# Kernel optimization log

Measured on AMD Instinct MI355X. Metric: run time of the kernel, lower is better.

The kernel has to match this reference:

```python
import jax, jax.numpy as jnp
import numpy as np

STATE_DIM = 512
N_AGENTS = 16
N_ACTIONS = 32
EMBED = 512          # mixing_embed_dim
Q_IN = STATE_DIM + N_AGENTS * N_ACTIONS  # 1024 (coma_critic arch)
ROWS = 32768         # bs * ts = 64 * 512


def _linear_params(key, d_in, d_out):
    kw, kb = jax.random.split(key)
    bound = 1.0 / np.sqrt(d_in)
    W = jax.random.uniform(kw, (d_in, d_out), minval=-bound, maxval=bound, dtype=jnp.float32)
    b = jax.random.uniform(kb, (d_out,), minval=-bound, maxval=bound, dtype=jnp.float32)
    return W, b


def setup_inputs() -> dict:
    key = jax.random.key(0)
    ks = jax.random.split(key, 8)
    states = jax.random.normal(ks[0], (ROWS, STATE_DIM), dtype=jnp.float32)
    actions = jax.random.uniform(ks[1], (ROWS, N_AGENTS * N_ACTIONS), dtype=jnp.float32)
    Qw1, Qb1 = _linear_params(ks[2], Q_IN, EMBED)
    Qw2, Qb2 = _linear_params(ks[3], EMBED, EMBED)
    Qw3, Qb3 = _linear_params(ks[4], EMBED, 1)
    Vw1, Vb1 = _linear_params(ks[5], STATE_DIM, EMBED)
    Vw2, Vb2 = _linear_params(ks[6], EMBED, EMBED)
    Vw3, Vb3 = _linear_params(ks[7], EMBED, 1)
    return {
        "states": states, "actions": actions,
        "Qw1": Qw1, "Qb1": Qb1, "Qw2": Qw2, "Qb2": Qb2, "Qw3": Qw3, "Qb3": Qb3,
        "Vw1": Vw1, "Vb1": Vb1, "Vw2": Vw2, "Vb2": Vb2, "Vw3": Vw3, "Vb3": Vb3,
    }


def _mlp3(x, W1, b1, W2, b2, W3, b3):
    h = jax.nn.relu(x @ W1 + b1)
    h = jax.nn.relu(h @ W2 + b2)
    return h @ W3 + b3


def reference(states, actions,
              Qw1, Qb1, Qw2, Qb2, Qw3, Qb3,
              Vw1, Vb1, Vw2, Vb2, Vw3, Vb3):
    # coma_critic arch: inputs = cat([states, joint-action one-hots], dim=1)
    inputs = jnp.concatenate([states, actions], axis=1)  # [bs*ts, Q_IN]
    q_outputs = _mlp3(inputs, Qw1, Qb1, Qw2, Qb2, Qw3, Qb3)  # [bs*ts, 1]
    v_outputs = _mlp3(states, Vw1, Vb1, Vw2, Vb2, Vw3, Vb3)  # [bs*ts, 1]
    return q_outputs, v_outputs
```

## Files before the change

kernel.cpp:

```cpp
#include <hip/hip_runtime.h>


#define ROWS 32768
#define EMBED 512

using frag_ab = __attribute__((ext_vector_type(8))) short;
using f32x4   = __attribute__((ext_vector_type(4))) float;

__device__ __forceinline__ unsigned short f2bf(float f) {
    unsigned int u = __builtin_bit_cast(unsigned int, f);
    return (unsigned short)((u + 0x7fffu + ((u >> 16) & 1u)) >> 16);
}

__device__ __forceinline__ unsigned pk2rne(float lo, float hi) {
    return (unsigned)f2bf(lo) | ((unsigned)f2bf(hi) << 16);
}

__device__ __forceinline__ void async_copy16(const void* g, void* l) {
    __builtin_amdgcn_global_load_lds(
        (const __attribute__((address_space(1))) unsigned int*)g,
        (__attribute__((address_space(3))) unsigned int*)l, 16, 0, 0);
}

#define VM8()   asm volatile("s_waitcnt vmcnt(8)" ::: "memory")
#define VM4()   asm volatile("s_waitcnt vmcnt(4)" ::: "memory")
#define VM0()   asm volatile("s_waitcnt vmcnt(0)" ::: "memory")
#define SBAR()  __builtin_amdgcn_s_barrier()

__global__ __launch_bounds__(256)
void prep(const float* __restrict__ states, const float* __restrict__ actions,
          const float* __restrict__ Qw1, const float* __restrict__ Qw2,
          const float* __restrict__ Vw1, const float* __restrict__ Vw2,
          const float* __restrict__ qb3, const float* __restrict__ vb3,
          unsigned short* __restrict__ X,
          unsigned short* __restrict__ Qw1t, unsigned short* __restrict__ Qw2t,
          unsigned short* __restrict__ Vw1t, unsigned short* __restrict__ Vw2t,
          float* __restrict__ out) {
    const int b = blockIdx.x, tid = threadIdx.x;
    if (b < 16384) {
        int g = b * 256 + tid;
        int m = g >> 7, col = (g & 127) * 8;
        const float* src = (col < 512) ? states + (size_t)m * 512 + col
                                       : actions + (size_t)m * 512 + (col - 512);
        float4 f0 = ((const float4*)src)[0];
        float4 f1 = ((const float4*)src)[1];
        *(uint4*)(X + (size_t)m * 1024 + col) =
            make_uint4(pk2rne(f0.x, f0.y), pk2rne(f0.z, f0.w),
                       pk2rne(f1.x, f1.y), pk2rne(f1.z, f1.w));
    } else if (b < 16704) {
        __shared__ float T[64][65];
        int tg = b - 16384;
        const float* W; unsigned short* O; int Krows, kt, nt;
        if (tg < 128) { W = Qw1; O = Qw1t; Krows = 1024; kt = tg >> 3; nt = tg & 7; }
        else {
            tg -= 128; int seg = tg >> 6, r = tg & 63;
            kt = r >> 3; nt = r & 7; Krows = 512;
            W = (seg == 0) ? Qw2 : (seg == 1) ? Vw1 : Vw2;
            O = (seg == 0) ? Qw2t : (seg == 1) ? Vw1t : Vw2t;
        }
        const int k0 = kt * 64, n0 = nt * 64;
        const int rr = tid >> 4, c4 = (tid & 15) * 4;
#pragma unroll
        for (int p = 0; p < 4; ++p) {
            float4 v = *(const float4*)&W[(size_t)(k0 + p * 16 + rr) * 512 + n0 + c4];
            T[p * 16 + rr][c4]     = v.x;
            T[p * 16 + rr][c4 + 1] = v.y;
            T[p * 16 + rr][c4 + 2] = v.z;
            T[p * 16 + rr][c4 + 3] = v.w;
        }
        __syncthreads();
        const int n = tid >> 2, kc = (tid & 3) * 16;
        unsigned pk[8];
#pragma unroll
        for (int j = 0; j < 8; ++j)
            pk[j] = pk2rne(T[kc + 2 * j][n], T[kc + 2 * j + 1][n]);
        uint4* dst = (uint4*)(O + (size_t)(n0 + n) * Krows + k0 + kc);
        dst[0] = make_uint4(pk[0], pk[1], pk[2], pk[3]);
        dst[1] = make_uint4(pk[4], pk[5], pk[6], pk[7]);
    } else {
        int i = (b - 16704) * 256 + tid;
        out[i] = (i < ROWS) ? qb3[0] : vb3[0];
    }
}

__device__ __forceinline__ void gemm_k32(
    const unsigned short* __restrict__ A, int ldaE,
    const unsigned short* __restrict__ Bt, int ldbE,
    int NT, int bm, int bn, char* smb, f32x4 acc[8][4])
{
    const int tid = threadIdx.x, wave = tid >> 6, lane = tid & 63;
    const int im = wave >> 2, in = wave & 3;
    const int lrow = lane & 15, quad = lane >> 4;
    const size_t ldaB = (size_t)ldaE * 2, ldbB = (size_t)ldbE * 2;

    const int srow = wave * 32 + (lane >> 2);
    const int sk   = (lane & 3) * 16;
    const char* gA = (const char*)A + (size_t)(bm + srow) * ldaB + sk;
    const char* gB = (const char*)Bt + (size_t)(bn + srow) * ldbB + sk;
    char* ldsAw = smb + wave * 2048;
    char* ldsBw = smb + 65536 + wave * 2048;

    auto stage = [&](int t) {
        const int b = t & 3;
        const char* a  = gA + (size_t)t * 64;
        const char* bs = gB + (size_t)t * 64;
        async_copy16(a,             ldsAw + b * 16384);
        async_copy16(a + 16 * ldaB, ldsAw + b * 16384 + 1024);
        async_copy16(bs,             ldsBw + b * 16384);
        async_copy16(bs + 16 * ldbB, ldsBw + b * 16384 + 1024);
    };

    auto compute = [&](int t) {
        const char* baseA = smb + (t & 3) * 16384 + im * 8192;
        const char* baseB = smb + 65536 + (t & 3) * 16384 + in * 4096;
        frag_ab a[8], b[4];
#pragma unroll
        for (int i = 0; i < 8; ++i)
            a[i] = *(const frag_ab*)(baseA + (i * 16 + lrow) * 64 + quad * 16);
#pragma unroll
        for (int j = 0; j < 4; ++j)
            b[j] = *(const frag_ab*)(baseB + (j * 16 + lrow) * 64 + quad * 16);
        __builtin_amdgcn_s_setprio(1);
#pragma unroll
        for (int i = 0; i < 8; ++i)
#pragma unroll
            for (int j = 0; j < 4; ++j)
                acc[i][j] = __builtin_amdgcn_mfma_f32_16x16x32_bf16(
                    a[i], b[j], acc[i][j], 0, 0, 0);
        __builtin_amdgcn_s_setprio(0);
    };

    stage(0);
    if (NT > 1) stage(1);
    if (NT > 2) stage(2);

    for (int t = 0; t < NT; ++t) {
        if (t + 3 <= NT) VM8();
        else if (t + 2 <= NT) VM4();
        else VM0();
        SBAR();
        if (t + 3 < NT) stage(t + 3);
        compute(t);
    }
}

__device__ __forceinline__ void decode_work(int bid, bool& isV, int& mi, int& nh) {
    isV = bid >= 256;
    int r = bid & 255;
    int work = ((r & 7) << 5) | (r >> 3);
    mi = work >> 1; nh = work & 1;
}

__global__ __launch_bounds__(512, 2)
void layer1(const unsigned short* __restrict__ X,
            const unsigned short* __restrict__ Qw1t,
            const unsigned short* __restrict__ Vw1t,
            const float* __restrict__ Qb1, const float* __restrict__ Vb1,
            unsigned short* __restrict__ h1Q, unsigned short* __restrict__ h1V) {
    __shared__ __align__(16) char smem[131072];
    bool isV; int mi, nh; decode_work(blockIdx.x, isV, mi, nh);
    const int bm = mi * 256, bn = nh * 256;
    const int NT = isV ? 16 : 32;
    const unsigned short* Wt = isV ? Vw1t : Qw1t;
    const int ldb = isV ? 512 : 1024;
    const float* bias = isV ? Vb1 : Qb1;
    unsigned short* H = isV ? h1V : h1Q;

    f32x4 acc[8][4] = {};
    gemm_k32(X, 1024, Wt, ldb, NT, bm, bn, smem, acc);

    const int tid = threadIdx.x, wave = tid >> 6, lane = tid & 63;
    const int im = wave >> 2, in = wave & 3;
    const int lrow = lane & 15, quad = lane >> 4;
#pragma unroll
    for (int j = 0; j < 4; ++j) {
        const int col = bn + in * 64 + j * 16 + lrow;
        const float bc = bias[col];
#pragma unroll
        for (int i = 0; i < 8; ++i) {
            const int row0 = bm + im * 128 + i * 16 + quad * 4;
#pragma unroll
            for (int r = 0; r < 4; ++r) {
                float val = acc[i][j][r] + bc;
                val = val > 0.0f ? val : 0.0f;
                H[(size_t)(row0 + r) * EMBED + col] = f2bf(val);
            }
        }
    }
}

__global__ __launch_bounds__(512, 2)
void layer2(const unsigned short* __restrict__ h1Q,
            const unsigned short* __restrict__ h1V,
            const unsigned short* __restrict__ Qw2t,
            const unsigned short* __restrict__ Vw2t,
            const float* __restrict__ Qb2, const float* __restrict__ Vb2,
            const float* __restrict__ Qw3, const float* __restrict__ Vw3,
            float* __restrict__ out) {
    __shared__ __align__(16) char smem[131072];
    bool isV; int mi, nh; decode_work(blockIdx.x, isV, mi, nh);
    const int bm = mi * 256, bn = nh * 256;
    const unsigned short* A  = isV ? h1V : h1Q;
    const unsigned short* Wt = isV ? Vw2t : Qw2t;
    const float* bias = isV ? Vb2 : Qb2;
    const float* w3   = isV ? Vw3 : Qw3;
    float* op = out + (isV ? ROWS : 0);

    f32x4 acc[8][4] = {};
    gemm_k32(A, 512, Wt, 512, 16, bm, bn, smem, acc);

    const int tid = threadIdx.x, wave = tid >> 6, lane = tid & 63;
    const int im = wave >> 2, in = wave & 3;
    const int lrow = lane & 15, quad = lane >> 4;
    float bc[4], wc[4];
#pragma unroll
    for (int j = 0; j < 4; ++j) {
        const int col = bn + in * 64 + j * 16 + lrow;
        bc[j] = bias[col];
        wc[j] = w3[col];
    }
#pragma unroll
    for (int i = 0; i < 8; ++i) {
#pragma unroll
        for (int r = 0; r < 4; ++r) {
            float s = 0.0f;
#pragma unroll
            for (int j = 0; j < 4; ++j) {
                float val = acc[i][j][r] + bc[j];
                val = val > 0.0f ? val : 0.0f;
                s += val * wc[j];
            }
#pragma unroll
            for (int m = 1; m < 16; m <<= 1) s += __shfl_xor(s, m, 64);
            if (lrow == 0)
                atomicAdd(&op[bm + im * 128 + i * 16 + quad * 4 + r], s);
        }
    }
}

extern "C" void kernel_launch(void* const* d_in, const int* in_sizes, int n_in,
                              void* d_out, int out_size, void* d_ws, size_t ws_size,
                              hipStream_t stream) {
    const float* states  = (const float*)d_in[0];
    const float* actions = (const float*)d_in[1];
    const float* Qw1 = (const float*)d_in[2];
    const float* Qb1 = (const float*)d_in[3];
    const float* Qw2 = (const float*)d_in[4];
    const float* Qb2 = (const float*)d_in[5];
    const float* Qw3 = (const float*)d_in[6];
    const float* Qb3 = (const float*)d_in[7];
    const float* Vw1 = (const float*)d_in[8];
    const float* Vb1 = (const float*)d_in[9];
    const float* Vw2 = (const float*)d_in[10];
    const float* Vb2 = (const float*)d_in[11];
    const float* Vw3 = (const float*)d_in[12];
    const float* Vb3 = (const float*)d_in[13];
    float* out = (float*)d_out;

    char* ws = (char*)d_ws;
    unsigned short* X    = (unsigned short*)ws;
    unsigned short* h1Q  = (unsigned short*)(ws + 67108864);
    unsigned short* h1V  = (unsigned short*)(ws + 100663296);
    unsigned short* Qw1t = (unsigned short*)(ws + 134217728);
    unsigned short* Qw2t = Qw1t + 512 * 1024;
    unsigned short* Vw1t = Qw2t + 512 * 512;
    unsigned short* Vw2t = Vw1t + 512 * 512;

    prep<<<dim3(16960), dim3(256), 0, stream>>>(states, actions, Qw1, Qw2, Vw1, Vw2,
                                                Qb3, Vb3, X, Qw1t, Qw2t, Vw1t, Vw2t, out);

    layer1<<<dim3(512), dim3(512), 0, stream>>>(X, Qw1t, Vw1t, Qb1, Vb1, h1Q, h1V);
    layer2<<<dim3(512), dim3(512), 0, stream>>>(h1Q, h1V, Qw2t, Vw2t, Qb2, Vb2, Qw3, Vw3, out);
}
```

Measured before the change: 299.1 us.

## Fuse both MLP layers into one kernel keeping hidden activations in LDS

Replaces the separate layer1/layer2 kernels with one fused kernel per 128-row tile. Layer-1 output is written as bf16 into swizzled LDS and consumed directly by the layer-2 GEMM, with Q and V heads processed sequentially. This removes the global round trip of the hidden activations and a kernel launch. In exchange it drops the async global-to-LDS pipelined staging, so operands load straight from global into registers, and it halves the grid with one block per CU.

```diff
diff --git a/kernel.cpp b/kernel.cpp
--- a/kernel.cpp
+++ b/kernel.cpp
@@ -2,7 +2,6 @@
 
 
 #define ROWS 32768
-#define EMBED 512
 
 using frag_ab = __attribute__((ext_vector_type(8))) short;
 using f32x4   = __attribute__((ext_vector_type(4))) float;
@@ -15,17 +14,6 @@
 __device__ __forceinline__ unsigned pk2rne(float lo, float hi) {
     return (unsigned)f2bf(lo) | ((unsigned)f2bf(hi) << 16);
 }
-
-__device__ __forceinline__ void async_copy16(const void* g, void* l) {
-    __builtin_amdgcn_global_load_lds(
-        (const __attribute__((address_space(1))) unsigned int*)g,
-        (__attribute__((address_space(3))) unsigned int*)l, 16, 0, 0);
-}
-
-#define VM8()   asm volatile("s_waitcnt vmcnt(8)" ::: "memory")
-#define VM4()   asm volatile("s_waitcnt vmcnt(4)" ::: "memory")
-#define VM0()   asm volatile("s_waitcnt vmcnt(0)" ::: "memory")
-#define SBAR()  __builtin_amdgcn_s_barrier()
 
 __global__ __launch_bounds__(256)
 void prep(const float* __restrict__ states, const float* __restrict__ actions,
@@ -83,159 +71,149 @@
     }
 }
 
-__device__ __forceinline__ void gemm_k32(
-    const unsigned short* __restrict__ A, int ldaE,
-    const unsigned short* __restrict__ Bt, int ldbE,
-    int NT, int bm, int bn, char* smb, f32x4 acc[8][4])
-{
+__global__ __launch_bounds__(512, 2)
+void fused(const unsigned short* __restrict__ X,
+           const unsigned short* __restrict__ Qw1t,
+           const unsigned short* __restrict__ Vw1t,
+           const float* __restrict__ Qb1, const float* __restrict__ Vb1,
+           const unsigned short* __restrict__ Qw2t,
+           const unsigned short* __restrict__ Vw2t,
+           const float* __restrict__ Qb2, const float* __restrict__ Vb2,
+           const float* __restrict__ Qw3, const float* __restrict__ Vw3,
+           float* __restrict__ out) {
+    __shared__ __align__(16) char h1[131072];
     const int tid = threadIdx.x, wave = tid >> 6, lane = tid & 63;
     const int im = wave >> 2, in = wave & 3;
     const int lrow = lane & 15, quad = lane >> 4;
-    const size_t ldaB = (size_t)ldaE * 2, ldbB = (size_t)ldbE * 2;
-
-    const int srow = wave * 32 + (lane >> 2);
-    const int sk   = (lane & 3) * 16;
-    const char* gA = (const char*)A + (size_t)(bm + srow) * ldaB + sk;
-    const char* gB = (const char*)Bt + (size_t)(bn + srow) * ldbB + sk;
-    char* ldsAw = smb + wave * 2048;
-    char* ldsBw = smb + 65536 + wave * 2048;
-
-    auto stage = [&](int t) {
-        const int b = t & 3;
-        const char* a  = gA + (size_t)t * 64;
-        const char* bs = gB + (size_t)t * 64;
-        async_copy16(a,             ldsAw + b * 16384);
-        async_copy16(a + 16 * ldaB, ldsAw + b * 16384 + 1024);
-        async_copy16(bs,             ldsBw + b * 16384);
-        async_copy16(bs + 16 * ldbB, ldsBw + b * 16384 + 1024);
+    const int bid = blockIdx.x;
+    const int mi = ((bid & 7) << 5) | (bid >> 3);
+    const int bm = mi * 128;
+
+    auto l1 = [&](const unsigned short* Wt, int ldb, int NT, const float* bias) {
+#pragma unroll 1
+        for (int nt = 0; nt < 2; ++nt) {
+            f32x4 acc[4][4] = {};
+            const unsigned short* Ab =
+                X + (size_t)(bm + im * 64 + lrow) * 1024 + quad * 8;
+            const unsigned short* Bb =
+                Wt + (size_t)(nt * 256 + in * 64 + lrow) * ldb + quad * 8;
+#pragma unroll 2
+            for (int kt = 0; kt < NT; ++kt) {
+                frag_ab a[4][2], b[4][2];
+#pragma unroll
+                for (int i = 0; i < 4; ++i)
+#pragma unroll
+                    for (int s = 0; s < 2; ++s)
+                        a[i][s] = *(const frag_ab*)(Ab + (size_t)i * 16 * 1024 +
+                                                    kt * 64 + s * 32);
+#pragma unroll
+                for (int j = 0; j < 4; ++j)
+#pragma unroll
+                    for (int s = 0; s < 2; ++s)
+                        b[j][s] = *(const frag_ab*)(Bb + (size_t)j * 16 * ldb +
+                                                    kt * 64 + s * 32);
+#pragma unroll
+                for (int s = 0; s < 2; ++s)
+#pragma unroll
+                    for (int i = 0; i < 4; ++i)
+#pragma unroll
+                        for (int j = 0; j < 4; ++j)
+                            acc[i][j] = __builtin_amdgcn_mfma_f32_16x16x32_bf16(
+                                a[i][s], b[j][s], acc[i][j], 0, 0, 0);
+            }
+#pragma unroll
+            for (int j = 0; j < 4; ++j) {
+                const int col = nt * 256 + in * 64 + j * 16 + lrow;
+                const float bc = bias[col];
+#pragma unroll
+                for (int i = 0; i < 4; ++i)
+#pragma unroll
+                    for (int r = 0; r < 4; ++r) {
+                        float v = acc[i][j][r] + bc;
+                        v = v > 0.0f ? v : 0.0f;
+                        const int row = im * 64 + i * 16 + quad * 4 + r;
+                        const int u = (col >> 3) ^ (row & 7);
+                        *(unsigned short*)(h1 + row * 1024 + (u << 4) +
+                                           (col & 7) * 2) = f2bf(v);
+                    }
+            }
+        }
     };
 
-    auto compute = [&](int t) {
-        const char* baseA = smb + (t & 3) * 16384 + im * 8192;
-        const char* baseB = smb + 65536 + (t & 3) * 16384 + in * 4096;
-        frag_ab a[8], b[4];
-#pragma unroll
-        for (int i = 0; i < 8; ++i)
-            a[i] = *(const frag_ab*)(baseA + (i * 16 + lrow) * 64 + quad * 16);
-#pragma unroll
-        for (int j = 0; j < 4; ++j)
-            b[j] = *(const frag_ab*)(baseB + (j * 16 + lrow) * 64 + quad * 16);
-        __builtin_amdgcn_s_setprio(1);
-#pragma unroll
-        for (int i = 0; i < 8; ++i)
-#pragma unroll
-            for (int j = 0; j < 4; ++j)
-                acc[i][j] = __builtin_amdgcn_mfma_f32_16x16x32_bf16(
-                    a[i], b[j], acc[i][j], 0, 0, 0);
-        __builtin_amdgcn_s_setprio(0);
+    auto l2 = [&](const unsigned short* W2t, const float* b2,
+                  const float* w3, float* op) {
+        float ssum[4][4] = {};
+#pragma unroll 1
+        for (int nt = 0; nt < 2; ++nt) {
+            f32x4 acc[4][4] = {};
+            const unsigned short* Bb =
+                W2t + (size_t)(nt * 256 + in * 64 + lrow) * 512 + quad * 8;
+#pragma unroll 2
+            for (int kt = 0; kt < 8; ++kt) {
+                frag_ab a[4][2], b[4][2];
+#pragma unroll
+                for (int i = 0; i < 4; ++i)
+#pragma unroll
+                    for (int s = 0; s < 2; ++s) {
+                        const int row = im * 64 + i * 16 + lrow;
+                        const int u = (kt * 8 + s * 4 + quad) ^ (row & 7);
+                        a[i][s] = *(const frag_ab*)(h1 + row * 1024 + (u << 4));
+                    }
+#pragma unroll
+                for (int j = 0; j < 4; ++j)
+#pragma unroll
+                    for (int s = 0; s < 2; ++s)
+                        b[j][s] = *(const frag_ab*)(Bb + (size_t)j * 16 * 512 +
+                                                    kt * 64 + s * 32);
+#pragma unroll
+                for (int s = 0; s < 2; ++s)
+#pragma unroll
+                    for (int i = 0; i < 4; ++i)
+#pragma unroll
+                        for (int j = 0; j < 4; ++j)
+                            acc[i][j] = __builtin_amdgcn_mfma_f32_16x16x32_bf16(
+                                a[i][s], b[j][s], acc[i][j], 0, 0, 0);
+            }
+            float bc[4], wc[4];
+#pragma unroll
+            for (int j = 0; j < 4; ++j) {
+                const int col = nt * 256 + in * 64 + j * 16 + lrow;
+                bc[j] = b2[col];
+                wc[j] = w3[col];
+            }
+#pragma unroll
+            for (int i = 0; i < 4; ++i)
+#pragma unroll
+                for (int r = 0; r < 4; ++r) {
+                    float s = 0.0f;
+#pragma unroll
+                    for (int j = 0; j < 4; ++j) {
+                        float v = acc[i][j][r] + bc[j];
+                        v = v > 0.0f ? v : 0.0f;
+                        s += v * wc[j];
+                    }
+#pragma unroll
+                    for (int m = 1; m < 16; m <<= 1) s += __shfl_xor(s, m, 64);
+                    ssum[i][r] += s;
+                }
+        }
+        if (lrow == 0) {
+#pragma unroll
+            for (int i = 0; i < 4; ++i)
+#pragma unroll
+                for (int r = 0; r < 4; ++r)
+                    atomicAdd(&op[bm + im * 64 + i * 16 + quad * 4 + r],
+                              ssum[i][r]);
+        }
     };
 
-    stage(0);
-    if (NT > 1) stage(1);
-    if (NT > 2) stage(2);
-
-    for (int t = 0; t < NT; ++t) {
-        if (t + 3 <= NT) VM8();
-        else if (t + 2 <= NT) VM4();
-        else VM0();
-        SBAR();
-        if (t + 3 < NT) stage(t + 3);
-        compute(t);
-    }
-}
-
-__device__ __forceinline__ void decode_work(int bid, bool& isV, int& mi, int& nh) {
-    isV = bid >= 256;
-    int r = bid & 255;
-    int work = ((r & 7) << 5) | (r >> 3);
-    mi = work >> 1; nh = work & 1;
-}
-
-__global__ __launch_bounds__(512, 2)
-void layer1(const unsigned short* __restrict__ X,
-            const unsigned short* __restrict__ Qw1t,
-            const unsigned short* __restrict__ Vw1t,
-            const float* __restrict__ Qb1, const float* __restrict__ Vb1,
-            unsigned short* __restrict__ h1Q, unsigned short* __restrict__ h1V) {
-    __shared__ __align__(16) char smem[131072];
-    bool isV; int mi, nh; decode_work(blockIdx.x, isV, mi, nh);
-    const int bm = mi * 256, bn = nh * 256;
-    const int NT = isV ? 16 : 32;
-    const unsigned short* Wt = isV ? Vw1t : Qw1t;
-    const int ldb = isV ? 512 : 1024;
-    const float* bias = isV ? Vb1 : Qb1;
-    unsigned short* H = isV ? h1V : h1Q;
-
-    f32x4 acc[8][4] = {};
-    gemm_k32(X, 1024, Wt, ldb, NT, bm, bn, smem, acc);
-
-    const int tid = threadIdx.x, wave = tid >> 6, lane = tid & 63;
-    const int im = wave >> 2, in = wave & 3;
-    const int lrow = lane & 15, quad = lane >> 4;
-#pragma unroll
-    for (int j = 0; j < 4; ++j) {
-        const int col = bn + in * 64 + j * 16 + lrow;
-        const float bc = bias[col];
-#pragma unroll
-        for (int i = 0; i < 8; ++i) {
-            const int row0 = bm + im * 128 + i * 16 + quad * 4;
-#pragma unroll
-            for (int r = 0; r < 4; ++r) {
-                float val = acc[i][j][r] + bc;
-                val = val > 0.0f ? val : 0.0f;
-                H[(size_t)(row0 + r) * EMBED + col] = f2bf(val);
-            }
-        }
-    }
-}
-
-__global__ __launch_bounds__(512, 2)
-void layer2(const unsigned short* __restrict__ h1Q,
-            const unsigned short* __restrict__ h1V,
-            const unsigned short* __restrict__ Qw2t,
-            const unsigned short* __restrict__ Vw2t,
-            const float* __restrict__ Qb2, const float* __restrict__ Vb2,
-            const float* __restrict__ Qw3, const float* __restrict__ Vw3,
-            float* __restrict__ out) {
-    __shared__ __align__(16) char smem[131072];
-    bool isV; int mi, nh; decode_work(blockIdx.x, isV, mi, nh);
-    const int bm = mi * 256, bn = nh * 256;
-    const unsigned short* A  = isV ? h1V : h1Q;
-    const unsigned short* Wt = isV ? Vw2t : Qw2t;
-    const float* bias = isV ? Vb2 : Qb2;
-    const float* w3   = isV ? Vw3 : Qw3;
-    float* op = out + (isV ? ROWS : 0);
-
-    f32x4 acc[8][4] = {};
-    gemm_k32(A, 512, Wt, 512, 16, bm, bn, smem, acc);
-
-    const int tid = threadIdx.x, wave = tid >> 6, lane = tid & 63;
-    const int im = wave >> 2, in = wave & 3;
-    const int lrow = lane & 15, quad = lane >> 4;
-    float bc[4], wc[4];
-#pragma unroll
-    for (int j = 0; j < 4; ++j) {
-        const int col = bn + in * 64 + j * 16 + lrow;
-        bc[j] = bias[col];
-        wc[j] = w3[col];
-    }
-#pragma unroll
-    for (int i = 0; i < 8; ++i) {
-#pragma unroll
-        for (int r = 0; r < 4; ++r) {
-            float s = 0.0f;
-#pragma unroll
-            for (int j = 0; j < 4; ++j) {
-                float val = acc[i][j][r] + bc[j];
-                val = val > 0.0f ? val : 0.0f;
-                s += val * wc[j];
-            }
-#pragma unroll
-            for (int m = 1; m < 16; m <<= 1) s += __shfl_xor(s, m, 64);
-            if (lrow == 0)
-                atomicAdd(&op[bm + im * 128 + i * 16 + quad * 4 + r], s);
-        }
-    }
+    l1(Qw1t, 1024, 16, Qb1);
+    __syncthreads();
+    l2(Qw2t, Qb2, Qw3, out);
+    __syncthreads();
+    l1(Vw1t, 512, 8, Vb1);
+    __syncthreads();
+    l2(Vw2t, Vb2, Vw3, out + ROWS);
 }
 
 extern "C" void kernel_launch(void* const* d_in, const int* in_sizes, int n_in,
@@ -259,9 +237,7 @@
 
     char* ws = (char*)d_ws;
     unsigned short* X    = (unsigned short*)ws;
-    unsigned short* h1Q  = (unsigned short*)(ws + 67108864);
-    unsigned short* h1V  = (unsigned short*)(ws + 100663296);
-    unsigned short* Qw1t = (unsigned short*)(ws + 134217728);
+    unsigned short* Qw1t = (unsigned short*)(ws + 67108864);
     unsigned short* Qw2t = Qw1t + 512 * 1024;
     unsigned short* Vw1t = Qw2t + 512 * 512;
     unsigned short* Vw2t = Vw1t + 512 * 512;
@@ -269,6 +245,6 @@
     prep<<<dim3(16960), dim3(256), 0, stream>>>(states, actions, Qw1, Qw2, Vw1, Vw2,
                                                 Qb3, Vb3, X, Qw1t, Qw2t, Vw1t, Vw2t, out);
 
-    layer1<<<dim3(512), dim3(512), 0, stream>>>(X, Qw1t, Vw1t, Qb1, Vb1, h1Q, h1V);
-    layer2<<<dim3(512), dim3(512), 0, stream>>>(h1Q, h1V, Qw2t, Vw2t, Qb2, Vb2, Qw3, Vw3, out);
-}
+    fused<<<dim3(256), dim3(512), 0, stream>>>(X, Qw1t, Vw1t, Qb1, Vb1,
+                                               Qw2t, Vw2t, Qb2, Vb2, Qw3, Vw3, out);
+}
```

Result: slower. 408.2 us (+36.5%).
